# Kernel tuning notes

Hardware: AMD Instinct MI355X
Metric: run time of the kernel (lower is better)

## Reference

```python
import jax, jax.numpy as jnp
import numpy as np

N, LATENT, HIDDEN, OUT, B = 65536, 128, 512, 64, 1024
W_WIDTH = 4.0  # LSH bucket width params['w']


def setup_inputs() -> dict:
    key = jax.random.key(0)
    ks = jax.random.split(key, 6)
    return {
        "z": jax.random.normal(ks[0], (N, LATENT), jnp.float32),
        "W1": jax.random.normal(ks[1], (LATENT, HIDDEN), jnp.float32) / np.float32(np.sqrt(LATENT)),
        "b1": jnp.zeros((HIDDEN,), jnp.float32),
        "W2": jax.random.normal(ks[2], (HIDDEN, OUT), jnp.float32) / np.float32(np.sqrt(HIDDEN)),
        "b2": jnp.zeros((OUT,), jnp.float32),
        "a": jax.random.normal(ks[3], (OUT,), jnp.float32),
        "lsh_b": jax.random.uniform(ks[4], (1,), jnp.float32) * W_WIDTH,
    }


def reference(z, W1, b1, W2, b2, a, lsh_b):
    # decoder MLP: latent -> hidden (relu) -> output_dim
    h = jax.nn.relu(z @ W1 + b1)
    x = h @ W2 + b2                                     # [N, OUT]
    # LSH random-projection hash: floor((x.a + b)/w), bucketed mod B
    code = jnp.floor((x @ a + lsh_b[0]) / W_WIDTH)
    bucket = jnp.mod(code.astype(jnp.int32), B)         # [N] segment ids
    # dict-based cluster grouping -> segmented mean per hash bucket
    sums = jax.ops.segment_sum(x, bucket, num_segments=B)                # [B, OUT]
    counts = jax.ops.segment_sum(jnp.ones((x.shape[0],), x.dtype), bucket, num_segments=B)
    means = sums / jnp.maximum(counts, 1.0)[:, None]    # [B, OUT]
    # squared distances point -> every cluster mean (gram trick, no [N,B,OUT] tensor)
    d2 = jnp.maximum(
        jnp.sum(x * x, -1)[:, None] + jnp.sum(means * means, -1)[None, :]
        - 2.0 * (x @ means.T),
        0.0)                                            # [N, B]
    # DEC-style Student-t soft cluster assignment
    q = 1.0 / (1.0 + d2)
    q_s = q / jnp.sum(q, -1, keepdims=True)
    return (q_s, means)
```

## Files before the change

kernel.cpp:

```cpp
#include <hip/hip_runtime.h>
#include <hip/hip_bf16.h>

#define N_PTS   65536
#define LATENT  128
#define HIDDEN  512
#define OUT_D   64
#define NBUCKET 1024
#define ROWS_A  32

typedef __attribute__((ext_vector_type(8))) short frag_ab;
typedef __attribute__((ext_vector_type(4))) float f32x4;

__device__ __forceinline__ short bf16h(float f) {
    union { float f; unsigned u; } c; c.f = f;
    const unsigned r = (c.u + 0x7FFFu + ((c.u >> 16) & 1u)) >> 16;
    return (short)r;
}
__device__ __forceinline__ float bf16tof(short s) {
    union { unsigned u; float f; } c; c.u = ((unsigned)(unsigned short)s) << 16;
    return c.f;
}

__global__ __launch_bounds__(256) void prep_weights(
    const float* __restrict__ W1, const float* __restrict__ W2,
    short* __restrict__ w1frag, short* __restrict__ w2frag)
{
    const int tid = blockIdx.x * 256 + threadIdx.x;
    if (tid < 32 * 64 * 4) {
        const int ct = tid >> 8, l = (tid >> 2) & 63, ks = tid & 3;
        const int n = ct * 16 + (l & 15);
        const int k0 = ks * 32 + ((l >> 4) << 3);
        frag_ab hi, lo;
#pragma unroll
        for (int e = 0; e < 8; ++e) {
            const float wv = W1[(size_t)(k0 + e) * HIDDEN + n];
            const short h = bf16h(wv);
            hi[e] = h;
            lo[e] = bf16h(wv - bf16tof(h));
        }
        frag_ab* dst = (frag_ab*)w1frag;
        const int u = ((ct * 64 + l) * 4 + ks) * 2;
        dst[u] = hi; dst[u + 1] = lo;
    } else {
        const int u0 = tid - 32 * 64 * 4;
        const int c = u0 >> 8, ot = (u0 >> 6) & 3, l = u0 & 63;
        const int n = ot * 16 + (l & 15);
        const int k0 = c * 32 + ((l >> 4) << 3);
        frag_ab hi, lo;
#pragma unroll
        for (int e = 0; e < 8; ++e) {
            const float wv = W2[(size_t)(k0 + e) * OUT_D + n];
            const short h = bf16h(wv);
            hi[e] = h;
            lo[e] = bf16h(wv - bf16tof(h));
        }
        frag_ab* dst = (frag_ab*)w2frag;
        const int u = ((c * 4 + ot) * 64 + l) * 2;
        dst[u] = hi; dst[u + 1] = lo;
    }
}

#define WB_UNITS 1728
#define W2_OFF   1152
#define H_OFF    3456
#define HW_UNITS 320
#define XP_STRIDE 512
#define BAND_U   5e-4f

__global__ __launch_bounds__(256, 2) void mlp_mfma_kernel(
    const float* __restrict__ z, const short* __restrict__ w1frag,
    const short* __restrict__ w2frag, const float* __restrict__ b1,
    const float* __restrict__ b2, const float* __restrict__ a,
    const float* __restrict__ lsh_b,
    short* __restrict__ xhi, short* __restrict__ xlo,
    float* __restrict__ xnorm_out, int* __restrict__ bucket_out,
    int* __restrict__ wsflag)
{
    __shared__ frag_ab LD[H_OFF + 4 * HW_UNITS];
    short* LDs = (short*)LD;
    const int t = threadIdx.x;
    const int l = t & 63, w = t >> 6;
    const int row0 = blockIdx.x * 128 + w * 32;

    frag_ab zh[2][4], zl[2][4];
#pragma unroll
    for (int rt = 0; rt < 2; ++rt)
#pragma unroll
        for (int ks = 0; ks < 4; ++ks) {
            const float* src = z + (size_t)(row0 + rt * 16 + (l & 15)) * LATENT
                             + ks * 32 + ((l >> 4) << 3);
            const float4 p0 = *(const float4*)src;
            const float4 p1 = *(const float4*)(src + 4);
            const float v[8] = {p0.x, p0.y, p0.z, p0.w, p1.x, p1.y, p1.z, p1.w};
#pragma unroll
            for (int e = 0; e < 8; ++e) {
                const short h = bf16h(v[e]);
                zh[rt][ks][e] = h;
                zl[rt][ks][e] = bf16h(v[e] - bf16tof(h));
            }
        }

    f32x4 acc2[2][4];
#pragma unroll
    for (int rt = 0; rt < 2; ++rt)
#pragma unroll
        for (int ot = 0; ot < 4; ++ot) acc2[rt][ot] = (f32x4){0.f, 0.f, 0.f, 0.f};

    const frag_ab* w1g = (const frag_ab*)w1frag;
    const frag_ab* w2g = (const frag_ab*)w2frag;
    const int hbase = H_OFF + w * HW_UNITS;

#pragma unroll
    for (int j = 0; j < 4; ++j) {
        const int i = t + 256 * j;
        LD[(i >> 9) * 576 + ((i >> 3) & 63) * 9 + (i & 7)] = w1g[i];
    }
#pragma unroll
    for (int j = 0; j < 2; ++j) {
        const int i = t + 256 * j;
        LD[W2_OFF + ((i >> 1) & 63) * 9 + (((i >> 7) << 1) | (i & 1))] = w2g[i];
    }
    __syncthreads();

#pragma unroll 1
    for (int c = 0; c < 16; ++c) {
        const int pb = (c & 1) * WB_UNITS;
        const int sb = WB_UNITS - pb;
        frag_ab st1[4], st2[2];
        if (c < 15) {
#pragma unroll
            for (int j = 0; j < 4; ++j) st1[j] = w1g[(c + 1) * 1024 + t + 256 * j];
#pragma unroll
            for (int j = 0; j < 2; ++j) st2[j] = w2g[(c + 1) * 512 + t + 256 * j];
        }
#pragma unroll
        for (int ct_l = 0; ct_l < 2; ++ct_l) {
            frag_ab bh[4], bl[4];
#pragma unroll
            for (int ks = 0; ks < 4; ++ks) {
                bh[ks] = LD[pb + ct_l * 576 + l * 9 + ks * 2];
                bl[ks] = LD[pb + ct_l * 576 + l * 9 + ks * 2 + 1];
            }
            const float b1v = b1[(c * 2 + ct_l) * 16 + (l & 15)];
            const int k_l = ct_l * 16 + (l & 15);
            const int gu = k_l >> 3, eu = k_l & 7;
#pragma unroll
            for (int rt = 0; rt < 2; ++rt) {
                f32x4 acc = (f32x4){0.f, 0.f, 0.f, 0.f};
#pragma unroll
                for (int ks = 0; ks < 4; ++ks) {
                    acc = __builtin_amdgcn_mfma_f32_16x16x32_bf16(zh[rt][ks], bh[ks], acc, 0, 0, 0);
                    acc = __builtin_amdgcn_mfma_f32_16x16x32_bf16(zh[rt][ks], bl[ks], acc, 0, 0, 0);
                    acc = __builtin_amdgcn_mfma_f32_16x16x32_bf16(zl[rt][ks], bh[ks], acc, 0, 0, 0);
                }
#pragma unroll
                for (int r = 0; r < 4; ++r) {
                    const float hv = fmaxf(acc[r] + b1v, 0.f);
                    const short hh = bf16h(hv);
                    const short hlo = bf16h(hv - bf16tof(hh));
                    const int row_l = rt * 16 + (l >> 4) * 4 + r;
                    LDs[(hbase + row_l * 5 + gu) * 8 + eu] = hh;
                    LDs[(hbase + 160 + row_l * 5 + gu) * 8 + eu] = hlo;
                }
            }
        }
        frag_ab ah[2], al[2];
#pragma unroll
        for (int rt = 0; rt < 2; ++rt) {
            const int row = rt * 16 + (l & 15);
            const int g = l >> 4;
            ah[rt] = LD[hbase + row * 5 + g];
            al[rt] = LD[hbase + 160 + row * 5 + g];
        }
#pragma unroll
        for (int ot = 0; ot < 4; ++ot) {
            const frag_ab b2h = LD[pb + W2_OFF + l * 9 + ot * 2];
            const frag_ab b2l = LD[pb + W2_OFF + l * 9 + ot * 2 + 1];
#pragma unroll
            for (int rt = 0; rt < 2; ++rt) {
                acc2[rt][ot] = __builtin_amdgcn_mfma_f32_16x16x32_bf16(ah[rt], b2h, acc2[rt][ot], 0, 0, 0);
                acc2[rt][ot] = __builtin_amdgcn_mfma_f32_16x16x32_bf16(ah[rt], b2l, acc2[rt][ot], 0, 0, 0);
                acc2[rt][ot] = __builtin_amdgcn_mfma_f32_16x16x32_bf16(al[rt], b2h, acc2[rt][ot], 0, 0, 0);
            }
        }
        if (c < 15) {
#pragma unroll
            for (int j = 0; j < 4; ++j) {
                const int i = t + 256 * j;
                LD[sb + (i >> 9) * 576 + ((i >> 3) & 63) * 9 + (i & 7)] = st1[j];
            }
#pragma unroll
            for (int j = 0; j < 2; ++j) {
                const int i = t + 256 * j;
                LD[sb + W2_OFF + ((i >> 1) & 63) * 9 + (((i >> 7) << 1) | (i & 1))] = st2[j];
            }
        }
        __syncthreads();
    }

    float b2v[4], av[4];
#pragma unroll
    for (int ot = 0; ot < 4; ++ot) {
        b2v[ot] = b2[ot * 16 + (l & 15)];
        av[ot]  = a[ot * 16 + (l & 15)];
    }
    const int pbase = w * XP_STRIDE;
    int flagged = 0;
    const float lb = lsh_b[0];
#pragma unroll
    for (int rt = 0; rt < 2; ++rt)
#pragma unroll
        for (int r = 0; r < 4; ++r) {
            float sp = 0.f, np = 0.f;
            const int row_l = rt * 16 + (l >> 4) * 4 + r;
#pragma unroll
            for (int ot = 0; ot < 4; ++ot) {
                const float xv = acc2[rt][ot][r] + b2v[ot];
                sp = fmaf(xv, av[ot], sp);
                np = fmaf(xv, xv, np);
                const int col = ot * 16 + (l & 15);
                const short xh = bf16h(xv);
                LDs[(pbase + row_l * 8 + (col >> 3)) * 8 + (col & 7)] = xh;
                LDs[(pbase + 256 + row_l * 8 + (col >> 3)) * 8 + (col & 7)] = bf16h(xv - bf16tof(xh));
            }
#pragma unroll
            for (int off = 8; off >= 1; off >>= 1) {
                sp += __shfl_xor(sp, off, 16);
                np += __shfl_xor(np, off, 16);
            }
            if ((l & 15) == 0) {
                const int row = row0 + row_l;
                const float v = sp + lb;
                const float u = v * 0.25f;
                const float fl = floorf(u);
                bucket_out[row] = ((int)fl) & (NBUCKET - 1);
                xnorm_out[row] = np;
                const float fr = u - fl;
                if (fr < BAND_U || fr > 1.f - BAND_U) flagged = 1;
            }
        }
    const unsigned long long fb = __ballot(flagged != 0);
    if (l == 0) wsflag[blockIdx.x * 4 + w] = (fb != 0ull) ? 1 : 0;

    frag_ab* xhi8 = (frag_ab*)xhi;
    frag_ab* xlo8 = (frag_ab*)xlo;
#pragma unroll
    for (int j = 0; j < 4; ++j) {
        const int u = l + 64 * j;
        const size_t gidx = (size_t)(row0 + (u >> 3)) * 8 + (u & 7);
        xhi8[gidx] = LD[pbase + u];
        xlo8[gidx] = LD[pbase + 256 + u];
    }
}

__global__ __launch_bounds__(256, 3) void mlp_fixup_kernel(
    const float* __restrict__ z, const float* __restrict__ W1,
    const float* __restrict__ b1, const float* __restrict__ W2,
    const float* __restrict__ b2, const float* __restrict__ a,
    const float* __restrict__ lsh_b, const int* __restrict__ wsflag,
    short* __restrict__ xhi, short* __restrict__ xlo,
    float* __restrict__ xnorm_out, int* __restrict__ bucket_out)
{
    if (wsflag[blockIdx.x] == 0) return;
    __shared__ float zt[ROWS_A][LATENT];
    __shared__ float ht[ROWS_A][256];
    const int t = threadIdx.x;
    const int row0 = blockIdx.x * ROWS_A;

    {
        const float4* z4 = reinterpret_cast<const float4*>(z + (size_t)row0 * LATENT);
        float4* zt4 = reinterpret_cast<float4*>(&zt[0][0]);
#pragma unroll
        for (int i = 0; i < 4; ++i) zt4[t + 256 * i] = z4[t + 256 * i];
    }
    __syncthreads();

    const int tx = t & 63, ty = t >> 6;
    const int txq = t & 31, tyq = t >> 5;

    float acc2[4][2];
#pragma unroll
    for (int i = 0; i < 4; ++i) { acc2[i][0] = 0.f; acc2[i][1] = 0.f; }

    for (int h = 0; h < 2; ++h) {
        float acc1[8][4];
#pragma unroll
        for (int i = 0; i < 8; ++i)
#pragma unroll
            for (int cc = 0; cc < 4; ++cc) acc1[i][cc] = 0.f;

        const int jbase = h * 256 + tx;
#pragma unroll 2
        for (int k = 0; k < LATENT; k += 4) {
            float wv[4][4];
#pragma unroll
            for (int kk = 0; kk < 4; ++kk)
#pragma unroll
                for (int cc = 0; cc < 4; ++cc)
                    wv[kk][cc] = W1[(size_t)(k + kk) * HIDDEN + jbase + 64 * cc];
            float4 zv[8];
#pragma unroll
            for (int i = 0; i < 8; ++i)
                zv[i] = *reinterpret_cast<const float4*>(&zt[ty * 8 + i][k]);
#pragma unroll
            for (int i = 0; i < 8; ++i)
#pragma unroll
                for (int cc = 0; cc < 4; ++cc) {
                    acc1[i][cc] = fmaf(zv[i].x, wv[0][cc], acc1[i][cc]);
                    acc1[i][cc] = fmaf(zv[i].y, wv[1][cc], acc1[i][cc]);
                    acc1[i][cc] = fmaf(zv[i].z, wv[2][cc], acc1[i][cc]);
                    acc1[i][cc] = fmaf(zv[i].w, wv[3][cc], acc1[i][cc]);
                }
        }
        float bb[4];
#pragma unroll
        for (int cc = 0; cc < 4; ++cc) bb[cc] = b1[jbase + 64 * cc];
#pragma unroll
        for (int i = 0; i < 8; ++i)
#pragma unroll
            for (int cc = 0; cc < 4; ++cc)
                ht[ty * 8 + i][tx + 64 * cc] = fmaxf(acc1[i][cc] + bb[cc], 0.f);
        __syncthreads();

#pragma unroll 2
        for (int k = 0; k < 256; k += 4) {
            float w2v[4][2];
#pragma unroll
            for (int kk = 0; kk < 4; ++kk) {
                w2v[kk][0] = W2[(size_t)(h * 256 + k + kk) * OUT_D + txq];
                w2v[kk][1] = W2[(size_t)(h * 256 + k + kk) * OUT_D + txq + 32];
            }
            float4 hv[4];
#pragma unroll
            for (int i = 0; i < 4; ++i)
                hv[i] = *reinterpret_cast<const float4*>(&ht[tyq * 4 + i][k]);
#pragma unroll
            for (int i = 0; i < 4; ++i)
#pragma unroll
                for (int cc = 0; cc < 2; ++cc) {
                    acc2[i][cc] = fmaf(hv[i].x, w2v[0][cc], acc2[i][cc]);
                    acc2[i][cc] = fmaf(hv[i].y, w2v[1][cc], acc2[i][cc]);
                    acc2[i][cc] = fmaf(hv[i].z, w2v[2][cc], acc2[i][cc]);
                    acc2[i][cc] = fmaf(hv[i].w, w2v[3][cc], acc2[i][cc]);
                }
        }
        __syncthreads();
    }

    const float bb0 = b2[txq], bb1 = b2[txq + 32];
    const float a0 = a[txq], a1 = a[txq + 32];
    const float lb = lsh_b[0];
#pragma unroll
    for (int i = 0; i < 4; ++i) {
        const int row = row0 + tyq * 4 + i;
        const float x0 = acc2[i][0] + bb0;
        const float x1 = acc2[i][1] + bb1;
        const short h0 = bf16h(x0), h1 = bf16h(x1);
        xhi[(size_t)row * OUT_D + txq]      = h0;
        xhi[(size_t)row * OUT_D + txq + 32] = h1;
        xlo[(size_t)row * OUT_D + txq]      = bf16h(x0 - bf16tof(h0));
        xlo[(size_t)row * OUT_D + txq + 32] = bf16h(x1 - bf16tof(h1));

        float sa = fmaf(x0, a0, x1 * a1);
        float sn = fmaf(x0, x0, x1 * x1);
#pragma unroll
        for (int off = 16; off >= 1; off >>= 1) {
            sa += __shfl_xor(sa, off, 32);
            sn += __shfl_xor(sn, off, 32);
        }
        if (txq == 0) {
            const float code = floorf((sa + lb) * 0.25f);
            bucket_out[row] = ((int)code) & (NBUCKET - 1);
            xnorm_out[row] = sn;
        }
    }
}

__global__ __launch_bounds__(256) void hist_kernel(
    const int* __restrict__ bucket, int* __restrict__ blockhist)
{
    __shared__ int h[NBUCKET];
    const int t = threadIdx.x, blk = blockIdx.x;
    for (int i = t; i < NBUCKET; i += 256) h[i] = 0;
    __syncthreads();
    const int rbase = blk * 1024;
#pragma unroll
    for (int i = 0; i < 4; ++i)
        atomicAdd(&h[bucket[rbase + i * 256 + t]], 1);
    __syncthreads();
    for (int i = t; i < NBUCKET; i += 256)
        blockhist[blk * NBUCKET + i] = h[i];
}

__global__ __launch_bounds__(1024) void scan_kernel(
    const int* __restrict__ blockhist, int* __restrict__ base,
    int* __restrict__ blockbase)
{
    __shared__ int sc[NBUCKET];
    const int b = threadIdx.x;
    int c = 0;
    for (int blk = 0; blk < 64; ++blk) c += blockhist[blk * NBUCKET + b];
    sc[b] = c;
    __syncthreads();
    for (int off = 1; off < NBUCKET; off <<= 1) {
        const int add = (b >= off) ? sc[b - off] : 0;
        __syncthreads();
        sc[b] += add;
        __syncthreads();
    }
    const int offset = sc[b] - c;
    base[b] = offset;
    if (b == NBUCKET - 1) base[NBUCKET] = offset + c;
    int run = offset;
    for (int blk = 0; blk < 64; ++blk) {
        blockbase[blk * NBUCKET + b] = run;
        run += blockhist[blk * NBUCKET + b];
    }
}

__global__ __launch_bounds__(256) void scatter_kernel(
    const int* __restrict__ bucket, const int* __restrict__ blockbase,
    int* __restrict__ order)
{
    __shared__ int lcur[NBUCKET];
    const int t = threadIdx.x, blk = blockIdx.x;
    for (int i = t; i < NBUCKET; i += 256) lcur[i] = 0;
    __syncthreads();
    const int rbase = blk * 1024;
#pragma unroll
    for (int i = 0; i < 4; ++i) {
        const int row = rbase + i * 256 + t;
        const int bk = bucket[row];
        const int r = atomicAdd(&lcur[bk], 1);
        order[blockbase[blk * NBUCKET + bk] + r] = row;
    }
}

__global__ __launch_bounds__(256) void chunksum_kernel(
    const short* __restrict__ xhi, const short* __restrict__ xlo,
    const int* __restrict__ order, const int* __restrict__ bucket,
    float* __restrict__ sums)
{
    const int t = threadIdx.x, lane = t & 63, w = t >> 6;
    const int c = blockIdx.x * 4 + w;
    const int i0 = c * 64;
    const int ordv = order[i0 + lane];
    const int bktv = bucket[ordv];
    float acc = 0.f;
    int cur = __shfl(bktv, 0, 64);
#pragma unroll 8
    for (int j = 0; j < 64; ++j) {
        const int rb = __shfl(ordv, j, 64);
        const int bb = __shfl(bktv, j, 64);
        if (bb != cur) {
            atomicAdd(&sums[(size_t)cur * OUT_D + lane], acc);
            acc = 0.f; cur = bb;
        }
        acc += bf16tof(xhi[(size_t)rb * OUT_D + lane])
             + bf16tof(xlo[(size_t)rb * OUT_D + lane]);
    }
    atomicAdd(&sums[(size_t)cur * OUT_D + lane], acc);
}

__global__ __launch_bounds__(64) void means_kernel(
    const float* __restrict__ sums, const int* __restrict__ base,
    float* __restrict__ means_out, float* __restrict__ mnorm,
    short* __restrict__ bfrag)
{
    const int b = blockIdx.x;
    const int k = threadIdx.x;
    const int cnt = base[b + 1] - base[b];
    const float m = sums[b * OUT_D + k] / fmaxf((float)cnt, 1.0f);
    means_out[b * OUT_D + k] = m;

    const short mh = bf16h(m);
    const short ml = bf16h(m - bf16tof(mh));
    const int tile = b >> 4, col = b & 15;
    const int lane = ((k & 31) >> 3) * 16 + col;
    const int f = (k >> 5) * 2;
    const size_t idx = ((size_t)(tile * 64 + lane) * 4 + f) * 8 + (k & 7);
    bfrag[idx] = mh;
    bfrag[idx + 8] = ml;

    float s = m * m;
#pragma unroll
    for (int off = 32; off >= 1; off >>= 1) s += __shfl_xor(s, off, 64);
    if (k == 0) mnorm[b] = s;
}

__global__ __launch_bounds__(256) void q_kernel(
    const short* __restrict__ xhi, const short* __restrict__ xlo,
    const float* __restrict__ xnorm, const short* __restrict__ bfrag,
    const float* __restrict__ mnorm, float* __restrict__ q_out)
{
    __shared__ float rs_lds[4][16];
    const int t = threadIdx.x;
    const int l = t & 63;
    const int w = t >> 6;
    const int row0 = blockIdx.x * 16;
    const int lrow = (l >> 4) * 4;
    const int lcol = l & 15;

    const frag_ab* xh8 = reinterpret_cast<const frag_ab*>(xhi);
    const frag_ab* xl8 = reinterpret_cast<const frag_ab*>(xlo);
    frag_ab ah[2], al[2];
#pragma unroll
    for (int kh = 0; kh < 2; ++kh) {
        const size_t idx8 = (size_t)(row0 + lcol) * 8 + kh * 4 + (l >> 4);
        ah[kh] = xh8[idx8];
        al[kh] = xl8[idx8];
    }

    float xn[4];
#pragma unroll
    for (int r = 0; r < 4; ++r) xn[r] = xnorm[row0 + lrow + r];

    const frag_ab* bf8 = reinterpret_cast<const frag_ab*>(bfrag);
    float qs[16][4];
    float rsp[4] = {0.f, 0.f, 0.f, 0.f};

#pragma unroll
    for (int j = 0; j < 16; ++j) {
        const int bt = w + 4 * j;
        const size_t bb = (size_t)(bt * 64 + l) * 4;
        const frag_ab b0h = bf8[bb + 0];
        const frag_ab b0l = bf8[bb + 1];
        const frag_ab b1h = bf8[bb + 2];
        const frag_ab b1l = bf8[bb + 3];

        f32x4 acc = {0.f, 0.f, 0.f, 0.f};
        acc = __builtin_amdgcn_mfma_f32_16x16x32_bf16(ah[0], b0h, acc, 0, 0, 0);
        acc = __builtin_amdgcn_mfma_f32_16x16x32_bf16(ah[1], b1h, acc, 0, 0, 0);
        acc = __builtin_amdgcn_mfma_f32_16x16x32_bf16(ah[0], b0l, acc, 0, 0, 0);
        acc = __builtin_amdgcn_mfma_f32_16x16x32_bf16(ah[1], b1l, acc, 0, 0, 0);
        acc = __builtin_amdgcn_mfma_f32_16x16x32_bf16(al[0], b0h, acc, 0, 0, 0);
        acc = __builtin_amdgcn_mfma_f32_16x16x32_bf16(al[1], b1h, acc, 0, 0, 0);

        const float mn = mnorm[bt * 16 + lcol];
#pragma unroll
        for (int r = 0; r < 4; ++r) {
            const float d2 = fmaxf(fmaf(-2.f, acc[r], xn[r] + mn), 0.f);
            const float qq = __builtin_amdgcn_rcpf(1.f + d2);
            qs[j][r] = qq;
            rsp[r] += qq;
        }
    }

#pragma unroll
    for (int off = 8; off >= 1; off >>= 1)
#pragma unroll
        for (int r = 0; r < 4; ++r) rsp[r] += __shfl_xor(rsp[r], off, 16);
    if (lcol == 0) {
#pragma unroll
        for (int r = 0; r < 4; ++r) rs_lds[w][lrow + r] = rsp[r];
    }
    __syncthreads();

    float inv[4];
#pragma unroll
    for (int r = 0; r < 4; ++r) {
        const float tot = rs_lds[0][lrow + r] + rs_lds[1][lrow + r]
                        + rs_lds[2][lrow + r] + rs_lds[3][lrow + r];
        inv[r] = __builtin_amdgcn_rcpf(tot);
    }

#pragma unroll
    for (int j = 0; j < 16; ++j) {
        const int col = (w + 4 * j) * 16 + lcol;
#pragma unroll
        for (int r = 0; r < 4; ++r)
            q_out[(size_t)(row0 + lrow + r) * NBUCKET + col] = qs[j][r] * inv[r];
    }
}

extern "C" void kernel_launch(void* const* d_in, const int* in_sizes, int n_in,
                              void* d_out, int out_size, void* d_ws, size_t ws_size,
                              hipStream_t stream) {
    const float* z    = (const float*)d_in[0];
    const float* W1   = (const float*)d_in[1];
    const float* b1   = (const float*)d_in[2];
    const float* W2   = (const float*)d_in[3];
    const float* b2   = (const float*)d_in[4];
    const float* a    = (const float*)d_in[5];
    const float* lshb = (const float*)d_in[6];

    float* q_out     = (float*)d_out;
    float* means_out = q_out + (size_t)N_PTS * NBUCKET;

    char* ws = (char*)d_ws;
    short* xhi    = (short*)ws;
    short* xlo    = xhi + (size_t)N_PTS * OUT_D;
    short* bfrag  = xlo + (size_t)N_PTS * OUT_D;
    short* w1frag = bfrag + (size_t)64 * 64 * 4 * 8;
    short* w2frag = w1frag + (size_t)32 * 64 * 8 * 8;
    float* xnorm  = (float*)(w2frag + (size_t)16 * 4 * 64 * 2 * 8);
    float* mnorm  = xnorm + N_PTS;
    float* sums   = mnorm + NBUCKET;
    int*   bucket = (int*)(sums + (size_t)NBUCKET * OUT_D);
    int*   order  = bucket + N_PTS;
    int*   blockhist = order + N_PTS;
    int*   blockbase = blockhist + 64 * NBUCKET;
    int*   base      = blockbase + 64 * NBUCKET;
    int*   wsflag    = base + NBUCKET + 1;

    hipMemsetAsync(sums, 0, (size_t)NBUCKET * OUT_D * sizeof(float), stream);

    prep_weights<<<48, 256, 0, stream>>>(W1, W2, w1frag, w2frag);
    mlp_mfma_kernel<<<N_PTS / 128, 256, 0, stream>>>(z, w1frag, w2frag, b1, b2, a, lshb,
                                                     xhi, xlo, xnorm, bucket, wsflag);
    mlp_fixup_kernel<<<N_PTS / ROWS_A, 256, 0, stream>>>(z, W1, b1, W2, b2, a, lshb, wsflag,
                                                         xhi, xlo, xnorm, bucket);
    hist_kernel<<<64, 256, 0, stream>>>(bucket, blockhist);
    scan_kernel<<<1, 1024, 0, stream>>>(blockhist, base, blockbase);
    scatter_kernel<<<64, 256, 0, stream>>>(bucket, blockbase, order);
    chunksum_kernel<<<256, 256, 0, stream>>>(xhi, xlo, order, bucket, sums);
    means_kernel<<<NBUCKET, 64, 0, stream>>>(sums, base, means_out, mnorm, bfrag);
    q_kernel<<<N_PTS / 16, 256, 0, stream>>>(xhi, xlo, xnorm, bfrag, mnorm, q_out);
}
```

Baseline: 257.0 us.

## Read MLP weight fragments directly from global memory and fold sums zeroing into hist

The MLP kernel no longer stages W1/W2 fragments in double-buffered shared memory. Each wave now loads its fragments straight from global memory, which are expected to stay resident in L2, and the per-chunk __syncthreads is dropped. This removes barrier and LDS staging overhead and shrinks the shared footprint, but weight-load latency is no longer hidden by a prefetch. Separately, the hipMemsetAsync of the segment sums is replaced by zeroing inside hist_kernel, saving one queued operation.

```diff
diff --git a/kernel.cpp b/kernel.cpp
--- a/kernel.cpp
+++ b/kernel.cpp
@@ -60,10 +60,6 @@
     }
 }
 
-#define WB_UNITS 1728
-#define W2_OFF   1152
-#define H_OFF    3456
-#define HW_UNITS 320
 #define XP_STRIDE 512
 #define BAND_U   5e-4f
 
@@ -76,11 +72,12 @@
     float* __restrict__ xnorm_out, int* __restrict__ bucket_out,
     int* __restrict__ wsflag)
 {
-    __shared__ frag_ab LD[H_OFF + 4 * HW_UNITS];
+    __shared__ frag_ab LD[4 * XP_STRIDE];
     short* LDs = (short*)LD;
     const int t = threadIdx.x;
     const int l = t & 63, w = t >> 6;
     const int row0 = blockIdx.x * 128 + w * 32;
+    const int hbase = w * XP_STRIDE;
 
     frag_ab zh[2][4], zl[2][4];
 #pragma unroll
@@ -108,38 +105,17 @@
 
     const frag_ab* w1g = (const frag_ab*)w1frag;
     const frag_ab* w2g = (const frag_ab*)w2frag;
-    const int hbase = H_OFF + w * HW_UNITS;
-
-#pragma unroll
-    for (int j = 0; j < 4; ++j) {
-        const int i = t + 256 * j;
-        LD[(i >> 9) * 576 + ((i >> 3) & 63) * 9 + (i & 7)] = w1g[i];
-    }
-#pragma unroll
-    for (int j = 0; j < 2; ++j) {
-        const int i = t + 256 * j;
-        LD[W2_OFF + ((i >> 1) & 63) * 9 + (((i >> 7) << 1) | (i & 1))] = w2g[i];
-    }
-    __syncthreads();
 
 #pragma unroll 1
     for (int c = 0; c < 16; ++c) {
-        const int pb = (c & 1) * WB_UNITS;
-        const int sb = WB_UNITS - pb;
-        frag_ab st1[4], st2[2];
-        if (c < 15) {
-#pragma unroll
-            for (int j = 0; j < 4; ++j) st1[j] = w1g[(c + 1) * 1024 + t + 256 * j];
-#pragma unroll
-            for (int j = 0; j < 2; ++j) st2[j] = w2g[(c + 1) * 512 + t + 256 * j];
-        }
 #pragma unroll
         for (int ct_l = 0; ct_l < 2; ++ct_l) {
+            const size_t wb = (size_t)c * 1024 + ct_l * 512 + l * 8;
             frag_ab bh[4], bl[4];
 #pragma unroll
             for (int ks = 0; ks < 4; ++ks) {
-                bh[ks] = LD[pb + ct_l * 576 + l * 9 + ks * 2];
-                bl[ks] = LD[pb + ct_l * 576 + l * 9 + ks * 2 + 1];
+                bh[ks] = w1g[wb + ks * 2];
+                bl[ks] = w1g[wb + ks * 2 + 1];
             }
             const float b1v = b1[(c * 2 + ct_l) * 16 + (l & 15)];
             const int k_l = ct_l * 16 + (l & 15);
@@ -174,8 +150,9 @@
         }
 #pragma unroll
         for (int ot = 0; ot < 4; ++ot) {
-            const frag_ab b2h = LD[pb + W2_OFF + l * 9 + ot * 2];
-            const frag_ab b2l = LD[pb + W2_OFF + l * 9 + ot * 2 + 1];
+            const size_t wb2 = (size_t)c * 512 + ot * 128 + l * 2;
+            const frag_ab b2h = w2g[wb2];
+            const frag_ab b2l = w2g[wb2 + 1];
 #pragma unroll
             for (int rt = 0; rt < 2; ++rt) {
                 acc2[rt][ot] = __builtin_amdgcn_mfma_f32_16x16x32_bf16(ah[rt], b2h, acc2[rt][ot], 0, 0, 0);
@@ -183,19 +160,6 @@
                 acc2[rt][ot] = __builtin_amdgcn_mfma_f32_16x16x32_bf16(al[rt], b2h, acc2[rt][ot], 0, 0, 0);
             }
         }
-        if (c < 15) {
-#pragma unroll
-            for (int j = 0; j < 4; ++j) {
-                const int i = t + 256 * j;
-                LD[sb + (i >> 9) * 576 + ((i >> 3) & 63) * 9 + (i & 7)] = st1[j];
-            }
-#pragma unroll
-            for (int j = 0; j < 2; ++j) {
-                const int i = t + 256 * j;
-                LD[sb + W2_OFF + ((i >> 1) & 63) * 9 + (((i >> 7) << 1) | (i & 1))] = st2[j];
-            }
-        }
-        __syncthreads();
     }
 
     float b2v[4], av[4];
@@ -377,11 +341,13 @@
 }
 
 __global__ __launch_bounds__(256) void hist_kernel(
-    const int* __restrict__ bucket, int* __restrict__ blockhist)
+    const int* __restrict__ bucket, int* __restrict__ blockhist,
+    float* __restrict__ sums)
 {
     __shared__ int h[NBUCKET];
     const int t = threadIdx.x, blk = blockIdx.x;
     for (int i = t; i < NBUCKET; i += 256) h[i] = 0;
+    for (int i = t; i < NBUCKET; i += 256) sums[blk * NBUCKET + i] = 0.f;
     __syncthreads();
     const int rbase = blk * 1024;
 #pragma unroll
@@ -603,14 +569,12 @@
     int*   base      = blockbase + 64 * NBUCKET;
     int*   wsflag    = base + NBUCKET + 1;
 
-    hipMemsetAsync(sums, 0, (size_t)NBUCKET * OUT_D * sizeof(float), stream);
-
     prep_weights<<<48, 256, 0, stream>>>(W1, W2, w1frag, w2frag);
     mlp_mfma_kernel<<<N_PTS / 128, 256, 0, stream>>>(z, w1frag, w2frag, b1, b2, a, lshb,
                                                      xhi, xlo, xnorm, bucket, wsflag);
     mlp_fixup_kernel<<<N_PTS / ROWS_A, 256, 0, stream>>>(z, W1, b1, W2, b2, a, lshb, wsflag,
                                                          xhi, xlo, xnorm, bucket);
-    hist_kernel<<<64, 256, 0, stream>>>(bucket, blockhist);
+    hist_kernel<<<64, 256, 0, stream>>>(bucket, blockhist, sums);
     scan_kernel<<<1, 1024, 0, stream>>>(blockhist, base, blockbase);
     scatter_kernel<<<64, 256, 0, stream>>>(bucket, blockbase, order);
     chunksum_kernel<<<256, 256, 0, stream>>>(xhi, xlo, order, bucket, sums);
```

Result: slower. 286.2 us (+11.4%).
